# Kernel optimization log

Hardware: AMD Instinct MI355X
Metric: run time of the kernel (lower is better)

The kernel has to match this reference:

```python
import jax, jax.numpy as jnp
import numpy as np


def setup_inputs() -> dict:
    key = jax.random.key(0)
    ks = jax.random.split(key, 15)
    B, r, d, h, na = 64, 64, 2048, 64, 256
    x = jax.random.normal(ks[0], (B, d, na), dtype=jnp.float32)
    L = jax.random.randint(ks[1], (B, 2, na), 0, 2).astype(jnp.float32)
    p = lambda i, shp: jax.random.normal(ks[i], shp, dtype=jnp.float32)
    return {
        "x": x, "L": L,
        "Aq": p(2, (r, d)), "Ak": p(3, (r, d)), "Av": p(4, (r, d)),
        "Aq1": p(5, (r, r)), "Ak1": p(6, (r, r)), "Av1": p(7, (r, r)),
        "Aq5": p(8, (r, r)), "Ak5": p(9, (r, r)), "Av5": p(10, (r, r)),
        "Ao": p(11, (r, r)), "Ao1": p(12, (r, r)), "Ao5": p(13, (h, r)),
    }


def reference(x, L, Aq, Ak, Av, Aq1, Ak1, Av1, Aq5, Ak5, Av5, Ao, Ao1, Ao5):
    B, d, na = x.shape
    # numNeighbors: count of L[:,0,:] >= 1 per batch, +1 -> [B,1,1]
    numN = jnp.sum((L[:, 0, :] >= 1.0).astype(jnp.float32), axis=1)[:, None, None] + 1.0
    scale = jnp.sqrt(numN)  # [B,1,1]

    def attn(M, Wq, Wk, Wv):
        # M: [B, f, na]; Wq/Wk/Wv: [r, f]
        Q = jax.nn.sigmoid(jnp.einsum('rf,bfn->bnr', Wq, M))  # [B,na,r]
        K = jax.nn.sigmoid(jnp.einsum('rf,bfn->brn', Wk, M))  # [B,r,na]
        V = jax.nn.sigmoid(jnp.einsum('rf,bfn->bnr', Wv, M))  # [B,na,r]
        A = jax.nn.softmax(jnp.einsum('bnr,brm->bnm', Q, K) / scale, axis=2)
        return jnp.einsum('bnm,bmr->brn', A, V)  # [B,r,na]

    o = attn(x, Aq, Ak, Av)
    M = jax.nn.silu(jnp.einsum('sr,brn->bsn', Ao, o))
    o = attn(M, Aq1, Ak1, Av1)
    M = jax.nn.silu(jnp.einsum('sr,brn->bsn', Ao1, o))
    o = attn(M, Aq5, Ak5, Av5)
    M = jax.nn.silu(jnp.einsum('hr,brn->bhn', Ao5, o))  # [B,h,na]

    blk = d // na  # rows per block (8)
    def diagvec(i):
        # kron(sum-of-squares, ones(1,2)) == repeat each element twice -> [B, 2*na]
        return jnp.repeat(jnp.sum(M[:, i * blk:(i + 1) * blk, :] ** 2, axis=1), 2, axis=1)

    M11, M12, M21, M22 = diagvec(0), diagvec(1), diagvec(2), diagvec(3)
    Mpp = jnp.sum(M[:, 4 * blk:, :] ** 2, axis=1)  # [B, na]

    # q = x[:, :4, :].transpose(1,2).reshape(B, 4*na) (agent-major ordering)
    q = jnp.transpose(x[:, :4, :], (0, 2, 1)).reshape(B, 4 * na)
    q1, q2 = q[:, :2 * na], q[:, 2 * na:]
    # Block matrix [[diag(M11), diag(M12)], [diag(M21), diag(M22)]] quadratic form,
    # computed without materializing the [B, 4na, 4na] matrix.
    quad = jnp.sum(M11 * q1 * q1 + M12 * q1 * q2 + M21 * q2 * q1 + M22 * q2 * q2,
                   axis=1, keepdims=True)
    return quad + jnp.sum(Mpp, axis=1, keepdims=True)  # [B, 1]
```

## Files before the change

### kernel.cpp

```cpp
#include <hip/hip_runtime.h>
#include <stdint.h>

typedef _Float16 f16;
typedef f16 f16x8 __attribute__((ext_vector_type(8)));
typedef float f32x4 __attribute__((ext_vector_type(4)));

#define MFMA(a,b,c) __builtin_amdgcn_mfma_f32_16x16x32_f16(a, b, c, 0, 0, 0)

__device__ __forceinline__ float sigmoidf_(float z) { return 1.0f / (1.0f + __expf(-z)); }

__global__ void prep_kernel(const float* __restrict__ L,
    const float* __restrict__ Aq, const float* __restrict__ Ak, const float* __restrict__ Av,
    const float* __restrict__ Aq1, const float* __restrict__ Ak1, const float* __restrict__ Av1,
    const float* __restrict__ Aq5, const float* __restrict__ Ak5, const float* __restrict__ Av5,
    const float* __restrict__ Ao, const float* __restrict__ Ao1, const float* __restrict__ Ao5,
    float* __restrict__ scale, f16* __restrict__ Wcat, f16* __restrict__ Wsm,
    float* __restrict__ out)
{
  __shared__ float r4[4];
  int blk = blockIdx.x, t = threadIdx.x;
  if (blk < 64) {
    float v = (L[blk * 512 + t] >= 1.0f) ? 1.0f : 0.0f;
    #pragma unroll
    for (int off = 32; off; off >>= 1) v += __shfl_down(v, off);
    if ((t & 63) == 0) r4[t >> 6] = v;
    __syncthreads();
    if (t == 0) scale[blk] = sqrtf(r4[0] + r4[1] + r4[2] + r4[3] + 1.0f);
  } else if (blk < 160) {
    int base = (blk - 64) * 4096;
    for (int i = 0; i < 16; i++) {
      int idx = base + t + i * 256;
      int row = idx >> 11, col = idx & 2047;
      float v = (row < 64) ? Aq[row * 2048 + col]
              : (row < 128) ? Ak[(row - 64) * 2048 + col]
              : Av[(row - 128) * 2048 + col];
      Wcat[idx] = (f16)v;
    }
  } else if (blk < 169) {
    int j = blk - 160;
    const float* s = (j == 0) ? Aq1 : (j == 1) ? Ak1 : (j == 2) ? Av1 : (j == 3) ? Aq5
                   : (j == 4) ? Ak5 : (j == 5) ? Av5 : (j == 6) ? Ao : (j == 7) ? Ao1 : Ao5;
    for (int i = 0; i < 16; i++) { int idx = t + i * 256; Wsm[j * 4096 + idx] = (f16)s[idx]; }
  } else {
    if (t < 64) out[t] = 0.0f;
  }
}

__global__ __launch_bounds__(256) void qkv1_kernel(const float* __restrict__ x,
    const f16* __restrict__ Wcat, f16* __restrict__ Qt, f16* __restrict__ Kt,
    f16* __restrict__ Vg)
{
  int b = blockIdx.y, n0 = blockIdx.x * 32;
  int t = threadIdx.x, lane = t & 63, w = t >> 6;
  int l15 = lane & 15, q = lane >> 4;
  __shared__ f16 xt[32 * 72];
  __shared__ f16 wt[192 * 72];
  f32x4 acc[2][3] = {};
  const float* xb = x + (size_t)b * 524288 + n0;
  int tn = t & 31, fg = t >> 5;

  for (int f0 = 0; f0 < 2048; f0 += 64) {
    #pragma unroll
    for (int rep = 0; rep < 4; rep++) {
      int fl = fg * 8 + rep * 2;
      float a0 = xb[(size_t)(f0 + fl) * 256 + tn];
      float a1 = xb[(size_t)(f0 + fl + 1) * 256 + tn];
      uint32_t pk = (uint32_t)__builtin_bit_cast(uint16_t, (f16)a0)
                  | ((uint32_t)__builtin_bit_cast(uint16_t, (f16)a1) << 16);
      *(uint32_t*)&xt[tn * 72 + fl] = pk;
    }
    #pragma unroll
    for (int i = 0; i < 6; i++) {
      int id = t + i * 256, r = id >> 3, c = id & 7;
      *(uint4*)&wt[r * 72 + c * 8] = *(const uint4*)(Wcat + (size_t)r * 2048 + f0 + c * 8);
    }
    __syncthreads();
    #pragma unroll
    for (int ks = 0; ks < 2; ks++) {
      int k0 = ks * 32 + q * 8;
      f16x8 af[2], bf[3];
      af[0] = *(const f16x8*)&xt[l15 * 72 + k0];
      af[1] = *(const f16x8*)&xt[(16 + l15) * 72 + k0];
      #pragma unroll
      for (int j = 0; j < 3; j++) bf[j] = *(const f16x8*)&wt[((w * 3 + j) * 16 + l15) * 72 + k0];
      #pragma unroll
      for (int nt = 0; nt < 2; nt++)
        #pragma unroll
        for (int j = 0; j < 3; j++)
          acc[nt][j] = MFMA(af[nt], bf[j], acc[nt][j]);
    }
    __syncthreads();
  }
  #pragma unroll
  for (int nt = 0; nt < 2; nt++)
    #pragma unroll
    for (int j = 0; j < 3; j++) {
      int rr = (w * 3 + j) * 16 + l15;
      float s[4];
      #pragma unroll
      for (int reg = 0; reg < 4; reg++) s[reg] = sigmoidf_(acc[nt][j][reg]);
      int nbase = n0 + nt * 16 + q * 4;
      if (rr < 64) {
        #pragma unroll
        for (int reg = 0; reg < 4; reg++)
          Qt[(size_t)b * 16384 + (size_t)(nbase + reg) * 64 + rr] = (f16)s[reg];
      } else if (rr < 128) {
        #pragma unroll
        for (int reg = 0; reg < 4; reg++)
          Kt[(size_t)b * 16384 + (size_t)(nbase + reg) * 64 + (rr - 64)] = (f16)s[reg];
      } else {
        union { f16 h[4]; uint2 u; } pk;
        #pragma unroll
        for (int reg = 0; reg < 4; reg++) pk.h[reg] = (f16)s[reg];
        *(uint2*)(Vg + (size_t)b * 16384 + (size_t)(rr - 128) * 256 + nbase) = pk.u;
      }
    }
}

template<int LAYER>
__global__ __launch_bounds__(512) void attnB_kernel(const float* __restrict__ x,
    const float* __restrict__ scale, const f16* __restrict__ Wsm,
    const f16* __restrict__ Qtg, const f16* __restrict__ Ktg, const f16* __restrict__ Vgg,
    const f16* __restrict__ Min, f16* __restrict__ Mout, float* __restrict__ out)
{
  int g = blockIdx.x, b = blockIdx.y, n0 = g * 64;
  int t = threadIdx.x, lane = t & 63, w = t >> 6;
  int l15 = lane & 15, q = lane >> 4;
  __shared__ f16 KT[256 * 72];
  __shared__ f16 SM[256 * 72];
  __shared__ f16 VM[64 * 264];
  __shared__ f16 QT[64 * 72];
  __shared__ f16 OT[64 * 72];
  __shared__ float denomS[64];

  float sinv = 1.0f / scale[b];
  if (t < 64) denomS[t] = 0.0f;

  if (LAYER == 0) {
    const uint4* qs = (const uint4*)(Qtg + (size_t)b * 16384 + (size_t)n0 * 64);
    { int n = t >> 3, c = t & 7; *(uint4*)&QT[n * 72 + c * 8] = qs[t]; }
    const uint4* ks = (const uint4*)(Ktg + (size_t)b * 16384);
    const uint4* vs = (const uint4*)(Vgg + (size_t)b * 16384);
    #pragma unroll
    for (int i = 0; i < 4; i++) {
      int id = t + i * 512;
      int m = id >> 3, c = id & 7;
      *(uint4*)&KT[m * 72 + c * 8] = ks[id];
      int r = id >> 5, c2 = id & 31;
      *(uint4*)&VM[r * 264 + c2 * 8] = vs[id];
    }
  } else {
    const uint4* ms = (const uint4*)(Min + (size_t)b * 16384);
    #pragma unroll
    for (int i = 0; i < 4; i++) {
      int id = t + i * 512, m = id >> 3, c = id & 7;
      *(uint4*)&SM[m * 72 + c * 8] = ms[id];
    }
  }
  __syncthreads();

  const f16* Wq = Wsm + (size_t)(LAYER == 1 ? 0 : 3) * 4096;
  const f16* Wk = Wsm + (size_t)(LAYER == 1 ? 1 : 4) * 4096;
  const f16* Wv = Wsm + (size_t)(LAYER == 1 ? 2 : 5) * 4096;
  const f16* Wo = Wsm + (size_t)(LAYER == 0 ? 6 : (LAYER == 1 ? 7 : 8)) * 4096;

  if (LAYER > 0) {
    if (w < 4) {
      f16x8 bk[4][2];
      #pragma unroll
      for (int rt = 0; rt < 4; rt++) {
        bk[rt][0] = *(const f16x8*)(Wk + (rt * 16 + l15) * 64 + q * 8);
        bk[rt][1] = *(const f16x8*)(Wk + (rt * 16 + l15) * 64 + 32 + q * 8);
      }
      #pragma unroll
      for (int mi = 0; mi < 4; mi++) {
        int mt = w * 4 + mi;
        f16x8 a0 = *(const f16x8*)&SM[(mt * 16 + l15) * 72 + q * 8];
        f16x8 a1 = *(const f16x8*)&SM[(mt * 16 + l15) * 72 + 32 + q * 8];
        #pragma unroll
        for (int rt = 0; rt < 4; rt++) {
          f32x4 acc = {}; acc = MFMA(a0, bk[rt][0], acc); acc = MFMA(a1, bk[rt][1], acc);
          #pragma unroll
          for (int reg = 0; reg < 4; reg++)
            KT[(mt * 16 + q * 4 + reg) * 72 + rt * 16 + l15] = (f16)sigmoidf_(acc[reg]);
        }
      }
    } else {
      f16x8 av[4][2];
      #pragma unroll
      for (int rt = 0; rt < 4; rt++) {
        av[rt][0] = *(const f16x8*)(Wv + (rt * 16 + l15) * 64 + q * 8);
        av[rt][1] = *(const f16x8*)(Wv + (rt * 16 + l15) * 64 + 32 + q * 8);
      }
      #pragma unroll
      for (int mi = 0; mi < 4; mi++) {
        int mt = (w - 4) * 4 + mi;
        f16x8 b0 = *(const f16x8*)&SM[(mt * 16 + l15) * 72 + q * 8];
        f16x8 b1 = *(const f16x8*)&SM[(mt * 16 + l15) * 72 + 32 + q * 8];
        #pragma unroll
        for (int rt = 0; rt < 4; rt++) {
          f32x4 acc = {}; acc = MFMA(av[rt][0], b0, acc); acc = MFMA(av[rt][1], b1, acc);
          #pragma unroll
          for (int reg = 0; reg < 4; reg++)
            VM[(rt * 16 + q * 4 + reg) * 264 + mt * 16 + l15] = (f16)sigmoidf_(acc[reg]);
        }
      }
    }
    {
      int nt = w >> 1;
      f16x8 a0 = *(const f16x8*)&SM[(n0 + nt * 16 + l15) * 72 + q * 8];
      f16x8 a1 = *(const f16x8*)&SM[(n0 + nt * 16 + l15) * 72 + 32 + q * 8];
      #pragma unroll
      for (int j = 0; j < 2; j++) {
        int rt = (w & 1) * 2 + j;
        f16x8 b0 = *(const f16x8*)(Wq + (rt * 16 + l15) * 64 + q * 8);
        f16x8 b1 = *(const f16x8*)(Wq + (rt * 16 + l15) * 64 + 32 + q * 8);
        f32x4 acc = {}; acc = MFMA(a0, b0, acc); acc = MFMA(a1, b1, acc);
        #pragma unroll
        for (int reg = 0; reg < 4; reg++)
          QT[(nt * 16 + q * 4 + reg) * 72 + rt * 16 + l15] = (f16)sigmoidf_(acc[reg]);
      }
    }
    __syncthreads();
  }

  {
    int nt = w >> 1;
    f16x8 a0 = *(const f16x8*)&QT[(nt * 16 + l15) * 72 + q * 8];
    f16x8 a1 = *(const f16x8*)&QT[(nt * 16 + l15) * 72 + 32 + q * 8];
    float dsum[4] = {0.f, 0.f, 0.f, 0.f};
    #pragma unroll
    for (int mi = 0; mi < 8; mi++) {
      int mt = (w & 1) * 8 + mi;
      f16x8 b0 = *(const f16x8*)&KT[(mt * 16 + l15) * 72 + q * 8];
      f16x8 b1 = *(const f16x8*)&KT[(mt * 16 + l15) * 72 + 32 + q * 8];
      f32x4 acc = {}; acc = MFMA(a0, b0, acc); acc = MFMA(a1, b1, acc);
      #pragma unroll
      for (int reg = 0; reg < 4; reg++) {
        float e = __expf(acc[reg] * sinv);
        dsum[reg] += e;
        SM[(nt * 16 + q * 4 + reg) * 264 + mt * 16 + l15] = (f16)e;
      }
    }
    #pragma unroll
    for (int reg = 0; reg < 4; reg++) {
      #pragma unroll
      for (int mask = 1; mask < 16; mask <<= 1) dsum[reg] += __shfl_xor(dsum[reg], mask);
    }
    if (l15 == 0) {
      #pragma unroll
      for (int reg = 0; reg < 4; reg++) atomicAdd(&denomS[nt * 16 + q * 4 + reg], dsum[reg]);
    }
  }
  __syncthreads();

  {
    int nt = w >> 1;
    f32x4 oacc[2] = {};
    #pragma unroll
    for (int kc = 0; kc < 8; kc++) {
      f16x8 af = *(const f16x8*)&SM[(nt * 16 + l15) * 264 + kc * 32 + q * 8];
      #pragma unroll
      for (int j = 0; j < 2; j++) {
        int rt = (w & 1) * 2 + j;
        f16x8 bf = *(const f16x8*)&VM[(rt * 16 + l15) * 264 + kc * 32 + q * 8];
        oacc[j] = MFMA(af, bf, oacc[j]);
      }
    }
    #pragma unroll
    for (int j = 0; j < 2; j++) {
      int rt = (w & 1) * 2 + j;
      #pragma unroll
      for (int reg = 0; reg < 4; reg++) {
        int row = nt * 16 + q * 4 + reg;
        OT[row * 72 + rt * 16 + l15] = (f16)(oacc[j][reg] / denomS[row]);
      }
    }
  }
  __syncthreads();

  f16* Mst = QT;
  {
    int nt = w >> 1;
    f16x8 a0 = *(const f16x8*)&OT[(nt * 16 + l15) * 72 + q * 8];
    f16x8 a1 = *(const f16x8*)&OT[(nt * 16 + l15) * 72 + 32 + q * 8];
    #pragma unroll
    for (int j = 0; j < 2; j++) {
      int st = (w & 1) * 2 + j;
      f16x8 b0 = *(const f16x8*)(Wo + (st * 16 + l15) * 64 + q * 8);
      f16x8 b1 = *(const f16x8*)(Wo + (st * 16 + l15) * 64 + 32 + q * 8);
      f32x4 acc = {}; acc = MFMA(a0, b0, acc); acc = MFMA(a1, b1, acc);
      #pragma unroll
      for (int reg = 0; reg < 4; reg++) {
        float z = acc[reg];
        Mst[(nt * 16 + q * 4 + reg) * 64 + st * 16 + l15] = (f16)(z * sigmoidf_(z));
      }
    }
  }
  __syncthreads();

  if (LAYER < 2) {
    int row = t >> 3, c = t & 7;
    *(uint4*)(Mout + (size_t)b * 16384 + (size_t)(n0 + row) * 64 + c * 8)
        = *(const uint4*)&Mst[row * 64 + c * 8];
  } else {
    float contrib = 0.0f;
    if (t < 64) {
      int ntok = n0 + t;
      const f16* row = &Mst[t * 64];
      float d[4] = {0, 0, 0, 0}, pp = 0.0f;
      #pragma unroll
      for (int gg = 0; gg < 8; gg++) {
        f16x8 v = *(const f16x8*)(row + gg * 8);
        float ss = 0.0f;
        #pragma unroll
        for (int k = 0; k < 8; k++) { float f = (float)v[k]; ss += f * f; }
        if (gg < 4) d[gg] = ss; else pp += ss;
      }
      int np = ntok >> 1, c0 = (ntok & 1) * 2;
      const float* xb = x + (size_t)b * 524288 + (size_t)c0 * 256;
      float q1a = xb[np], q1b = xb[256 + np];
      float q2a = xb[128 + np], q2b = xb[384 + np];
      contrib = d[0] * (q1a * q1a + q1b * q1b)
              + (d[1] + d[2]) * (q1a * q2a + q1b * q2b)
              + d[3] * (q2a * q2a + q2b * q2b) + pp;
    }
    if (w == 0) {
      #pragma unroll
      for (int off = 32; off; off >>= 1) contrib += __shfl_down(contrib, off);
      if (lane == 0) atomicAdd(out + b, contrib);
    }
  }
}

extern "C" void kernel_launch(void* const* d_in, const int* in_sizes, int n_in,
                              void* d_out, int out_size, void* d_ws, size_t ws_size,
                              hipStream_t stream) {
  const float* x   = (const float*)d_in[0];
  const float* L   = (const float*)d_in[1];
  const float* Aq  = (const float*)d_in[2];
  const float* Ak  = (const float*)d_in[3];
  const float* Av  = (const float*)d_in[4];
  const float* Aq1 = (const float*)d_in[5];
  const float* Ak1 = (const float*)d_in[6];
  const float* Av1 = (const float*)d_in[7];
  const float* Aq5 = (const float*)d_in[8];
  const float* Ak5 = (const float*)d_in[9];
  const float* Av5 = (const float*)d_in[10];
  const float* Ao  = (const float*)d_in[11];
  const float* Ao1 = (const float*)d_in[12];
  const float* Ao5 = (const float*)d_in[13];

  char* ws = (char*)d_ws;
  float* scale = (float*)ws;
  f16* Wcat  = (f16*)(ws + 256);
  f16* Wsm   = (f16*)(ws + 786688);
  f16* Qtg   = (f16*)(ws + 860416);
  f16* Ktg   = (f16*)(ws + 2957568);
  f16* Vgg   = (f16*)(ws + 5054720);
  f16* MbufA = (f16*)(ws + 7151872);
  f16* MbufB = (f16*)(ws + 9249024);
  float* out = (float*)d_out;

  prep_kernel<<<170, 256, 0, stream>>>(L, Aq, Ak, Av, Aq1, Ak1, Av1,
                                       Aq5, Ak5, Av5, Ao, Ao1, Ao5, scale, Wcat, Wsm, out);
  qkv1_kernel<<<dim3(8, 64), 256, 0, stream>>>(x, Wcat, Qtg, Ktg, Vgg);
  attnB_kernel<0><<<dim3(4, 64), 512, 0, stream>>>(x, scale, Wsm, Qtg, Ktg, Vgg,
                                                   nullptr, MbufA, out);
  attnB_kernel<1><<<dim3(4, 64), 512, 0, stream>>>(x, scale, Wsm, Qtg, Ktg, Vgg,
                                                   MbufA, MbufB, out);
  attnB_kernel<2><<<dim3(4, 64), 512, 0, stream>>>(x, scale, Wsm, Qtg, Ktg, Vgg,
                                                   MbufB, nullptr, out);
}
```

Baseline: 272.1 us.

## Fuse three attention layers with per-batch grid barriers and LDS-free QKV GEMM

Merges the three per-layer attention launches into one persistent kernel that loops over layers and synchronises the four blocks of each batch through a global atomic counter with spin-waiting. Separately, the first QKV projection drops its shared-memory staging: weights are pre-permuted in the prep kernel into the MFMA fragment layout, and x is gathered directly into registers. This targets launch overhead and LDS/barrier costs. The trade-offs are reliance on all blocks being co-resident for the spin barrier, and less coalesced strided global loads of x.

```diff
diff --git a/kernel.cpp b/kernel.cpp
--- a/kernel.cpp
+++ b/kernel.cpp
@@ -14,8 +14,8 @@
     const float* __restrict__ Aq1, const float* __restrict__ Ak1, const float* __restrict__ Av1,
     const float* __restrict__ Aq5, const float* __restrict__ Ak5, const float* __restrict__ Av5,
     const float* __restrict__ Ao, const float* __restrict__ Ao1, const float* __restrict__ Ao5,
-    float* __restrict__ scale, f16* __restrict__ Wcat, f16* __restrict__ Wsm,
-    float* __restrict__ out)
+    float* __restrict__ scale, f16* __restrict__ Wopt, f16* __restrict__ Wsm,
+    float* __restrict__ out, unsigned int* __restrict__ flagg)
 {
   __shared__ float r4[4];
   int blk = blockIdx.x, t = threadIdx.x;
@@ -30,11 +30,12 @@
     int base = (blk - 64) * 4096;
     for (int i = 0; i < 16; i++) {
       int idx = base + t + i * 256;
-      int row = idx >> 11, col = idx & 2047;
-      float v = (row < 64) ? Aq[row * 2048 + col]
-              : (row < 128) ? Ak[(row - 64) * 2048 + col]
-              : Av[(row - 128) * 2048 + col];
-      Wcat[idx] = (f16)v;
+      int r = idx >> 11, k = idx & 2047;
+      float v = (r < 64) ? Aq[r * 2048 + k]
+              : (r < 128) ? Ak[(r - 64) * 2048 + k]
+              : Av[(r - 128) * 2048 + k];
+      int rt = r >> 4, lr = r & 15, kc = k >> 5, qq = (k >> 3) & 3, jj = k & 7;
+      Wopt[((rt * 64 + kc) * 16 + lr) * 32 + qq * 8 + jj] = (f16)v;
     }
   } else if (blk < 169) {
     int j = blk - 160;
@@ -43,54 +44,43 @@
     for (int i = 0; i < 16; i++) { int idx = t + i * 256; Wsm[j * 4096 + idx] = (f16)s[idx]; }
   } else {
     if (t < 64) out[t] = 0.0f;
+    else if (t < 128) flagg[t - 64] = 0u;
   }
 }
 
 __global__ __launch_bounds__(256) void qkv1_kernel(const float* __restrict__ x,
-    const f16* __restrict__ Wcat, f16* __restrict__ Qt, f16* __restrict__ Kt,
+    const f16* __restrict__ Wopt, f16* __restrict__ Qt, f16* __restrict__ Kt,
     f16* __restrict__ Vg)
 {
   int b = blockIdx.y, n0 = blockIdx.x * 32;
   int t = threadIdx.x, lane = t & 63, w = t >> 6;
   int l15 = lane & 15, q = lane >> 4;
-  __shared__ f16 xt[32 * 72];
-  __shared__ f16 wt[192 * 72];
   f32x4 acc[2][3] = {};
-  const float* xb = x + (size_t)b * 524288 + n0;
-  int tn = t & 31, fg = t >> 5;
-
-  for (int f0 = 0; f0 < 2048; f0 += 64) {
-    #pragma unroll
-    for (int rep = 0; rep < 4; rep++) {
-      int fl = fg * 8 + rep * 2;
-      float a0 = xb[(size_t)(f0 + fl) * 256 + tn];
-      float a1 = xb[(size_t)(f0 + fl + 1) * 256 + tn];
-      uint32_t pk = (uint32_t)__builtin_bit_cast(uint16_t, (f16)a0)
-                  | ((uint32_t)__builtin_bit_cast(uint16_t, (f16)a1) << 16);
-      *(uint32_t*)&xt[tn * 72 + fl] = pk;
-    }
-    #pragma unroll
-    for (int i = 0; i < 6; i++) {
-      int id = t + i * 256, r = id >> 3, c = id & 7;
-      *(uint4*)&wt[r * 72 + c * 8] = *(const uint4*)(Wcat + (size_t)r * 2048 + f0 + c * 8);
-    }
-    __syncthreads();
-    #pragma unroll
-    for (int ks = 0; ks < 2; ks++) {
-      int k0 = ks * 32 + q * 8;
-      f16x8 af[2], bf[3];
-      af[0] = *(const f16x8*)&xt[l15 * 72 + k0];
-      af[1] = *(const f16x8*)&xt[(16 + l15) * 72 + k0];
-      #pragma unroll
-      for (int j = 0; j < 3; j++) bf[j] = *(const f16x8*)&wt[((w * 3 + j) * 16 + l15) * 72 + k0];
-      #pragma unroll
-      for (int nt = 0; nt < 2; nt++)
-        #pragma unroll
-        for (int j = 0; j < 3; j++)
-          acc[nt][j] = MFMA(af[nt], bf[j], acc[nt][j]);
-    }
-    __syncthreads();
+  const float* xb0 = x + (size_t)b * 524288 + n0 + l15;
+  const float* xb1 = xb0 + 16;
+  const f16* wb = Wopt + ((size_t)(w * 3) * 1024 + l15) * 32 + q * 8;
+
+  #pragma unroll 2
+  for (int kc = 0; kc < 64; kc++) {
+    int f = kc * 32 + q * 8;
+    const float* p0 = xb0 + (size_t)f * 256;
+    const float* p1 = xb1 + (size_t)f * 256;
+    f16x8 af0, af1;
+    #pragma unroll
+    for (int j = 0; j < 8; j++) af0[j] = (f16)p0[j * 256];
+    #pragma unroll
+    for (int j = 0; j < 8; j++) af1[j] = (f16)p1[j * 256];
+    f16x8 bf[3];
+    #pragma unroll
+    for (int j = 0; j < 3; j++)
+      bf[j] = *(const f16x8*)(wb + (size_t)j * 32768 + kc * 512);
+    #pragma unroll
+    for (int j = 0; j < 3; j++) {
+      acc[0][j] = MFMA(af0, bf[j], acc[0][j]);
+      acc[1][j] = MFMA(af1, bf[j], acc[1][j]);
+    }
   }
+
   #pragma unroll
   for (int nt = 0; nt < 2; nt++)
     #pragma unroll
@@ -117,11 +107,11 @@
     }
 }
 
-template<int LAYER>
-__global__ __launch_bounds__(512) void attnB_kernel(const float* __restrict__ x,
+__global__ __launch_bounds__(512) void attn_fused(const float* __restrict__ x,
     const float* __restrict__ scale, const f16* __restrict__ Wsm,
     const f16* __restrict__ Qtg, const f16* __restrict__ Ktg, const f16* __restrict__ Vgg,
-    const f16* __restrict__ Min, f16* __restrict__ Mout, float* __restrict__ out)
+    f16* __restrict__ MA, f16* __restrict__ MB,
+    unsigned int* __restrict__ flagg, float* __restrict__ out)
 {
   int g = blockIdx.x, b = blockIdx.y, n0 = g * 64;
   int t = threadIdx.x, lane = t & 63, w = t >> 6;
@@ -134,201 +124,214 @@
   __shared__ float denomS[64];
 
   float sinv = 1.0f / scale[b];
-  if (t < 64) denomS[t] = 0.0f;
-
-  if (LAYER == 0) {
-    const uint4* qs = (const uint4*)(Qtg + (size_t)b * 16384 + (size_t)n0 * 64);
-    { int n = t >> 3, c = t & 7; *(uint4*)&QT[n * 72 + c * 8] = qs[t]; }
-    const uint4* ks = (const uint4*)(Ktg + (size_t)b * 16384);
-    const uint4* vs = (const uint4*)(Vgg + (size_t)b * 16384);
-    #pragma unroll
-    for (int i = 0; i < 4; i++) {
-      int id = t + i * 512;
-      int m = id >> 3, c = id & 7;
-      *(uint4*)&KT[m * 72 + c * 8] = ks[id];
-      int r = id >> 5, c2 = id & 31;
-      *(uint4*)&VM[r * 264 + c2 * 8] = vs[id];
-    }
-  } else {
-    const uint4* ms = (const uint4*)(Min + (size_t)b * 16384);
-    #pragma unroll
-    for (int i = 0; i < 4; i++) {
-      int id = t + i * 512, m = id >> 3, c = id & 7;
-      *(uint4*)&SM[m * 72 + c * 8] = ms[id];
-    }
-  }
-  __syncthreads();
-
-  const f16* Wq = Wsm + (size_t)(LAYER == 1 ? 0 : 3) * 4096;
-  const f16* Wk = Wsm + (size_t)(LAYER == 1 ? 1 : 4) * 4096;
-  const f16* Wv = Wsm + (size_t)(LAYER == 1 ? 2 : 5) * 4096;
-  const f16* Wo = Wsm + (size_t)(LAYER == 0 ? 6 : (LAYER == 1 ? 7 : 8)) * 4096;
-
-  if (LAYER > 0) {
-    if (w < 4) {
-      f16x8 bk[4][2];
-      #pragma unroll
-      for (int rt = 0; rt < 4; rt++) {
-        bk[rt][0] = *(const f16x8*)(Wk + (rt * 16 + l15) * 64 + q * 8);
-        bk[rt][1] = *(const f16x8*)(Wk + (rt * 16 + l15) * 64 + 32 + q * 8);
-      }
-      #pragma unroll
-      for (int mi = 0; mi < 4; mi++) {
-        int mt = w * 4 + mi;
-        f16x8 a0 = *(const f16x8*)&SM[(mt * 16 + l15) * 72 + q * 8];
-        f16x8 a1 = *(const f16x8*)&SM[(mt * 16 + l15) * 72 + 32 + q * 8];
+
+  #pragma unroll 1
+  for (int l = 0; l < 3; l++) {
+    if (t < 64) denomS[t] = 0.0f;
+
+    const f16* Wq = Wsm + (size_t)(l == 1 ? 0 : 3) * 4096;
+    const f16* Wk = Wsm + (size_t)(l == 1 ? 1 : 4) * 4096;
+    const f16* Wv = Wsm + (size_t)(l == 1 ? 2 : 5) * 4096;
+    const f16* Wo = Wsm + (size_t)(l == 0 ? 6 : (l == 1 ? 7 : 8)) * 4096;
+
+    if (l == 0) {
+      const uint4* qs = (const uint4*)(Qtg + (size_t)b * 16384 + (size_t)n0 * 64);
+      { int n = t >> 3, c = t & 7; *(uint4*)&QT[n * 72 + c * 8] = qs[t]; }
+      const uint4* ks = (const uint4*)(Ktg + (size_t)b * 16384);
+      const uint4* vs = (const uint4*)(Vgg + (size_t)b * 16384);
+      #pragma unroll
+      for (int i = 0; i < 4; i++) {
+        int id = t + i * 512;
+        int m = id >> 3, c = id & 7;
+        *(uint4*)&KT[m * 72 + c * 8] = ks[id];
+        int r = id >> 5, c2 = id & 31;
+        *(uint4*)&VM[r * 264 + c2 * 8] = vs[id];
+      }
+      __syncthreads();
+    } else {
+      const f16* Min = (l == 1) ? MA : MB;
+      const uint4* ms = (const uint4*)(Min + (size_t)b * 16384);
+      #pragma unroll
+      for (int i = 0; i < 4; i++) {
+        int id = t + i * 512, m = id >> 3, c = id & 7;
+        *(uint4*)&SM[m * 72 + c * 8] = ms[id];
+      }
+      __syncthreads();
+      if (w < 4) {
+        f16x8 bk[4][2];
         #pragma unroll
         for (int rt = 0; rt < 4; rt++) {
-          f32x4 acc = {}; acc = MFMA(a0, bk[rt][0], acc); acc = MFMA(a1, bk[rt][1], acc);
+          bk[rt][0] = *(const f16x8*)(Wk + (rt * 16 + l15) * 64 + q * 8);
+          bk[rt][1] = *(const f16x8*)(Wk + (rt * 16 + l15) * 64 + 32 + q * 8);
+        }
+        #pragma unroll
+        for (int mi = 0; mi < 4; mi++) {
+          int mt = w * 4 + mi;
+          f16x8 a0 = *(const f16x8*)&SM[(mt * 16 + l15) * 72 + q * 8];
+          f16x8 a1 = *(const f16x8*)&SM[(mt * 16 + l15) * 72 + 32 + q * 8];
+          #pragma unroll
+          for (int rt = 0; rt < 4; rt++) {
+            f32x4 acc = {}; acc = MFMA(a0, bk[rt][0], acc); acc = MFMA(a1, bk[rt][1], acc);
+            #pragma unroll
+            for (int reg = 0; reg < 4; reg++)
+              KT[(mt * 16 + q * 4 + reg) * 72 + rt * 16 + l15] = (f16)sigmoidf_(acc[reg]);
+          }
+        }
+      } else {
+        f16x8 av[4][2];
+        #pragma unroll
+        for (int rt = 0; rt < 4; rt++) {
+          av[rt][0] = *(const f16x8*)(Wv + (rt * 16 + l15) * 64 + q * 8);
+          av[rt][1] = *(const f16x8*)(Wv + (rt * 16 + l15) * 64 + 32 + q * 8);
+        }
+        #pragma unroll
+        for (int mi = 0; mi < 4; mi++) {
+          int mt = (w - 4) * 4 + mi;
+          f16x8 b0 = *(const f16x8*)&SM[(mt * 16 + l15) * 72 + q * 8];
+          f16x8 b1 = *(const f16x8*)&SM[(mt * 16 + l15) * 72 + 32 + q * 8];
+          #pragma unroll
+          for (int rt = 0; rt < 4; rt++) {
+            f32x4 acc = {}; acc = MFMA(av[rt][0], b0, acc); acc = MFMA(av[rt][1], b1, acc);
+            #pragma unroll
+            for (int reg = 0; reg < 4; reg++)
+              VM[(rt * 16 + q * 4 + reg) * 264 + mt * 16 + l15] = (f16)sigmoidf_(acc[reg]);
+          }
+        }
+      }
+      {
+        int nt = w >> 1;
+        f16x8 a0 = *(const f16x8*)&SM[(n0 + nt * 16 + l15) * 72 + q * 8];
+        f16x8 a1 = *(const f16x8*)&SM[(n0 + nt * 16 + l15) * 72 + 32 + q * 8];
+        #pragma unroll
+        for (int j = 0; j < 2; j++) {
+          int rt = (w & 1) * 2 + j;
+          f16x8 b0 = *(const f16x8*)(Wq + (rt * 16 + l15) * 64 + q * 8);
+          f16x8 b1 = *(const f16x8*)(Wq + (rt * 16 + l15) * 64 + 32 + q * 8);
+          f32x4 acc = {}; acc = MFMA(a0, b0, acc); acc = MFMA(a1, b1, acc);
           #pragma unroll
           for (int reg = 0; reg < 4; reg++)
-            KT[(mt * 16 + q * 4 + reg) * 72 + rt * 16 + l15] = (f16)sigmoidf_(acc[reg]);
-        }
-      }
-    } else {
-      f16x8 av[4][2];
-      #pragma unroll
-      for (int rt = 0; rt < 4; rt++) {
-        av[rt][0] = *(const f16x8*)(Wv + (rt * 16 + l15) * 64 + q * 8);
-        av[rt][1] = *(const f16x8*)(Wv + (rt * 16 + l15) * 64 + 32 + q * 8);
-      }
-      #pragma unroll
-      for (int mi = 0; mi < 4; mi++) {
-        int mt = (w - 4) * 4 + mi;
-        f16x8 b0 = *(const f16x8*)&SM[(mt * 16 + l15) * 72 + q * 8];
-        f16x8 b1 = *(const f16x8*)&SM[(mt * 16 + l15) * 72 + 32 + q * 8];
-        #pragma unroll
-        for (int rt = 0; rt < 4; rt++) {
-          f32x4 acc = {}; acc = MFMA(av[rt][0], b0, acc); acc = MFMA(av[rt][1], b1, acc);
-          #pragma unroll
-          for (int reg = 0; reg < 4; reg++)
-            VM[(rt * 16 + q * 4 + reg) * 264 + mt * 16 + l15] = (f16)sigmoidf_(acc[reg]);
-        }
-      }
-    }
+            QT[(nt * 16 + q * 4 + reg) * 72 + rt * 16 + l15] = (f16)sigmoidf_(acc[reg]);
+        }
+      }
+      __syncthreads();
+    }
+
     {
       int nt = w >> 1;
-      f16x8 a0 = *(const f16x8*)&SM[(n0 + nt * 16 + l15) * 72 + q * 8];
-      f16x8 a1 = *(const f16x8*)&SM[(n0 + nt * 16 + l15) * 72 + 32 + q * 8];
+      f16x8 a0 = *(const f16x8*)&QT[(nt * 16 + l15) * 72 + q * 8];
+      f16x8 a1 = *(const f16x8*)&QT[(nt * 16 + l15) * 72 + 32 + q * 8];
+      float dsum[4] = {0.f, 0.f, 0.f, 0.f};
+      #pragma unroll
+      for (int mi = 0; mi < 8; mi++) {
+        int mt = (w & 1) * 8 + mi;
+        f16x8 b0 = *(const f16x8*)&KT[(mt * 16 + l15) * 72 + q * 8];
+        f16x8 b1 = *(const f16x8*)&KT[(mt * 16 + l15) * 72 + 32 + q * 8];
+        f32x4 acc = {}; acc = MFMA(a0, b0, acc); acc = MFMA(a1, b1, acc);
+        #pragma unroll
+        for (int reg = 0; reg < 4; reg++) {
+          float e = __expf(acc[reg] * sinv);
+          dsum[reg] += e;
+          SM[(nt * 16 + q * 4 + reg) * 264 + mt * 16 + l15] = (f16)e;
+        }
+      }
+      #pragma unroll
+      for (int reg = 0; reg < 4; reg++) {
+        #pragma unroll
+        for (int mask = 1; mask < 16; mask <<= 1) dsum[reg] += __shfl_xor(dsum[reg], mask);
+      }
+      if (l15 == 0) {
+        #pragma unroll
+        for (int reg = 0; reg < 4; reg++) atomicAdd(&denomS[nt * 16 + q * 4 + reg], dsum[reg]);
+      }
+    }
+    __syncthreads();
+
+    {
+      int nt = w >> 1;
+      f32x4 oacc[2] = {};
+      #pragma unroll
+      for (int kc = 0; kc < 8; kc++) {
+        f16x8 af = *(const f16x8*)&SM[(nt * 16 + l15) * 264 + kc * 32 + q * 8];
+        #pragma unroll
+        for (int j = 0; j < 2; j++) {
+          int rt = (w & 1) * 2 + j;
+          f16x8 bf = *(const f16x8*)&VM[(rt * 16 + l15) * 264 + kc * 32 + q * 8];
+          oacc[j] = MFMA(af, bf, oacc[j]);
+        }
+      }
       #pragma unroll
       for (int j = 0; j < 2; j++) {
         int rt = (w & 1) * 2 + j;
-        f16x8 b0 = *(const f16x8*)(Wq + (rt * 16 + l15) * 64 + q * 8);
-        f16x8 b1 = *(const f16x8*)(Wq + (rt * 16 + l15) * 64 + 32 + q * 8);
+        #pragma unroll
+        for (int reg = 0; reg < 4; reg++) {
+          int row = nt * 16 + q * 4 + reg;
+          OT[row * 72 + rt * 16 + l15] = (f16)(oacc[j][reg] / denomS[row]);
+        }
+      }
+    }
+    __syncthreads();
+
+    f16* Mst = QT;
+    {
+      int nt = w >> 1;
+      f16x8 a0 = *(const f16x8*)&OT[(nt * 16 + l15) * 72 + q * 8];
+      f16x8 a1 = *(const f16x8*)&OT[(nt * 16 + l15) * 72 + 32 + q * 8];
+      #pragma unroll
+      for (int j = 0; j < 2; j++) {
+        int st = (w & 1) * 2 + j;
+        f16x8 b0 = *(const f16x8*)(Wo + (st * 16 + l15) * 64 + q * 8);
+        f16x8 b1 = *(const f16x8*)(Wo + (st * 16 + l15) * 64 + 32 + q * 8);
         f32x4 acc = {}; acc = MFMA(a0, b0, acc); acc = MFMA(a1, b1, acc);
         #pragma unroll
-        for (int reg = 0; reg < 4; reg++)
-          QT[(nt * 16 + q * 4 + reg) * 72 + rt * 16 + l15] = (f16)sigmoidf_(acc[reg]);
+        for (int reg = 0; reg < 4; reg++) {
+          float z = acc[reg];
+          Mst[(nt * 16 + q * 4 + reg) * 64 + st * 16 + l15] = (f16)(z * sigmoidf_(z));
+        }
       }
     }
     __syncthreads();
-  }
-
-  {
-    int nt = w >> 1;
-    f16x8 a0 = *(const f16x8*)&QT[(nt * 16 + l15) * 72 + q * 8];
-    f16x8 a1 = *(const f16x8*)&QT[(nt * 16 + l15) * 72 + 32 + q * 8];
-    float dsum[4] = {0.f, 0.f, 0.f, 0.f};
-    #pragma unroll
-    for (int mi = 0; mi < 8; mi++) {
-      int mt = (w & 1) * 8 + mi;
-      f16x8 b0 = *(const f16x8*)&KT[(mt * 16 + l15) * 72 + q * 8];
-      f16x8 b1 = *(const f16x8*)&KT[(mt * 16 + l15) * 72 + 32 + q * 8];
-      f32x4 acc = {}; acc = MFMA(a0, b0, acc); acc = MFMA(a1, b1, acc);
-      #pragma unroll
-      for (int reg = 0; reg < 4; reg++) {
-        float e = __expf(acc[reg] * sinv);
-        dsum[reg] += e;
-        SM[(nt * 16 + q * 4 + reg) * 264 + mt * 16 + l15] = (f16)e;
-      }
-    }
-    #pragma unroll
-    for (int reg = 0; reg < 4; reg++) {
-      #pragma unroll
-      for (int mask = 1; mask < 16; mask <<= 1) dsum[reg] += __shfl_xor(dsum[reg], mask);
-    }
-    if (l15 == 0) {
-      #pragma unroll
-      for (int reg = 0; reg < 4; reg++) atomicAdd(&denomS[nt * 16 + q * 4 + reg], dsum[reg]);
-    }
-  }
-  __syncthreads();
-
-  {
-    int nt = w >> 1;
-    f32x4 oacc[2] = {};
-    #pragma unroll
-    for (int kc = 0; kc < 8; kc++) {
-      f16x8 af = *(const f16x8*)&SM[(nt * 16 + l15) * 264 + kc * 32 + q * 8];
-      #pragma unroll
-      for (int j = 0; j < 2; j++) {
-        int rt = (w & 1) * 2 + j;
-        f16x8 bf = *(const f16x8*)&VM[(rt * 16 + l15) * 264 + kc * 32 + q * 8];
-        oacc[j] = MFMA(af, bf, oacc[j]);
-      }
-    }
-    #pragma unroll
-    for (int j = 0; j < 2; j++) {
-      int rt = (w & 1) * 2 + j;
-      #pragma unroll
-      for (int reg = 0; reg < 4; reg++) {
-        int row = nt * 16 + q * 4 + reg;
-        OT[row * 72 + rt * 16 + l15] = (f16)(oacc[j][reg] / denomS[row]);
-      }
-    }
-  }
-  __syncthreads();
-
-  f16* Mst = QT;
-  {
-    int nt = w >> 1;
-    f16x8 a0 = *(const f16x8*)&OT[(nt * 16 + l15) * 72 + q * 8];
-    f16x8 a1 = *(const f16x8*)&OT[(nt * 16 + l15) * 72 + 32 + q * 8];
-    #pragma unroll
-    for (int j = 0; j < 2; j++) {
-      int st = (w & 1) * 2 + j;
-      f16x8 b0 = *(const f16x8*)(Wo + (st * 16 + l15) * 64 + q * 8);
-      f16x8 b1 = *(const f16x8*)(Wo + (st * 16 + l15) * 64 + 32 + q * 8);
-      f32x4 acc = {}; acc = MFMA(a0, b0, acc); acc = MFMA(a1, b1, acc);
-      #pragma unroll
-      for (int reg = 0; reg < 4; reg++) {
-        float z = acc[reg];
-        Mst[(nt * 16 + q * 4 + reg) * 64 + st * 16 + l15] = (f16)(z * sigmoidf_(z));
-      }
-    }
-  }
-  __syncthreads();
-
-  if (LAYER < 2) {
-    int row = t >> 3, c = t & 7;
-    *(uint4*)(Mout + (size_t)b * 16384 + (size_t)(n0 + row) * 64 + c * 8)
-        = *(const uint4*)&Mst[row * 64 + c * 8];
-  } else {
-    float contrib = 0.0f;
-    if (t < 64) {
-      int ntok = n0 + t;
-      const f16* row = &Mst[t * 64];
-      float d[4] = {0, 0, 0, 0}, pp = 0.0f;
-      #pragma unroll
-      for (int gg = 0; gg < 8; gg++) {
-        f16x8 v = *(const f16x8*)(row + gg * 8);
-        float ss = 0.0f;
-        #pragma unroll
-        for (int k = 0; k < 8; k++) { float f = (float)v[k]; ss += f * f; }
-        if (gg < 4) d[gg] = ss; else pp += ss;
-      }
-      int np = ntok >> 1, c0 = (ntok & 1) * 2;
-      const float* xb = x + (size_t)b * 524288 + (size_t)c0 * 256;
-      float q1a = xb[np], q1b = xb[256 + np];
-      float q2a = xb[128 + np], q2b = xb[384 + np];
-      contrib = d[0] * (q1a * q1a + q1b * q1b)
-              + (d[1] + d[2]) * (q1a * q2a + q1b * q2b)
-              + d[3] * (q2a * q2a + q2b * q2b) + pp;
-    }
-    if (w == 0) {
-      #pragma unroll
-      for (int off = 32; off; off >>= 1) contrib += __shfl_down(contrib, off);
-      if (lane == 0) atomicAdd(out + b, contrib);
+
+    if (l < 2) {
+      f16* Mout = (l == 0) ? MA : MB;
+      int row = t >> 3, c = t & 7;
+      *(uint4*)(Mout + (size_t)b * 16384 + (size_t)(n0 + row) * 64 + c * 8)
+          = *(const uint4*)&Mst[row * 64 + c * 8];
+      if (t == 0) {
+        __threadfence();
+        atomicAdd(&flagg[b], 1u);
+        unsigned int target = 4u * (unsigned)(l + 1);
+        while (__hip_atomic_load(&flagg[b], __ATOMIC_ACQUIRE, __HIP_MEMORY_SCOPE_AGENT) < target)
+          __builtin_amdgcn_s_sleep(2);
+        __threadfence();
+      }
+      __syncthreads();
+    } else {
+      float contrib = 0.0f;
+      if (t < 64) {
+        int ntok = n0 + t;
+        const f16* row = &Mst[t * 64];
+        float d[4] = {0, 0, 0, 0}, pp = 0.0f;
+        #pragma unroll
+        for (int gg = 0; gg < 8; gg++) {
+          f16x8 v = *(const f16x8*)(row + gg * 8);
+          float ss = 0.0f;
+          #pragma unroll
+          for (int k = 0; k < 8; k++) { float f = (float)v[k]; ss += f * f; }
+          if (gg < 4) d[gg] = ss; else pp += ss;
+        }
+        int np = ntok >> 1, c0 = (ntok & 1) * 2;
+        const float* xb = x + (size_t)b * 524288 + (size_t)c0 * 256;
+        float q1a = xb[np], q1b = xb[256 + np];
+        float q2a = xb[128 + np], q2b = xb[384 + np];
+        contrib = d[0] * (q1a * q1a + q1b * q1b)
+                + (d[1] + d[2]) * (q1a * q2a + q1b * q2b)
+                + d[3] * (q2a * q2a + q2b * q2b) + pp;
+      }
+      if (w == 0) {
+        #pragma unroll
+        for (int off = 32; off; off >>= 1) contrib += __shfl_down(contrib, off);
+        if (lane == 0) atomicAdd(out + b, contrib);
+      }
     }
   }
 }
@@ -353,22 +356,20 @@
 
   char* ws = (char*)d_ws;
   float* scale = (float*)ws;
-  f16* Wcat  = (f16*)(ws + 256);
+  f16* Wopt  = (f16*)(ws + 256);
   f16* Wsm   = (f16*)(ws + 786688);
   f16* Qtg   = (f16*)(ws + 860416);
   f16* Ktg   = (f16*)(ws + 2957568);
   f16* Vgg   = (f16*)(ws + 5054720);
   f16* MbufA = (f16*)(ws + 7151872);
   f16* MbufB = (f16*)(ws + 9249024);
+  unsigned int* flagg = (unsigned int*)(ws + 11346176);
   float* out = (float*)d_out;
 
   prep_kernel<<<170, 256, 0, stream>>>(L, Aq, Ak, Av, Aq1, Ak1, Av1,
-                                       Aq5, Ak5, Av5, Ao, Ao1, Ao5, scale, Wcat, Wsm, out);
-  qkv1_kernel<<<dim3(8, 64), 256, 0, stream>>>(x, Wcat, Qtg, Ktg, Vgg);
-  attnB_kernel<0><<<dim3(4, 64), 512, 0, stream>>>(x, scale, Wsm, Qtg, Ktg, Vgg,
-                                                   nullptr, MbufA, out);
-  attnB_kernel<1><<<dim3(4, 64), 512, 0, stream>>>(x, scale, Wsm, Qtg, Ktg, Vgg,
-                                                   MbufA, MbufB, out);
-  attnB_kernel<2><<<dim3(4, 64), 512, 0, stream>>>(x, scale, Wsm, Qtg, Ktg, Vgg,
-                                                   MbufB, nullptr, out);
+                                       Aq5, Ak5, Av5, Ao, Ao1, Ao5,
+                                       scale, Wopt, Wsm, out, flagg);
+  qkv1_kernel<<<dim3(8, 64), 256, 0, stream>>>(x, Wopt, Qtg, Ktg, Vgg);
+  attn_fused<<<dim3(4, 64), 512, 0, stream>>>(x, scale, Wsm, Qtg, Ktg, Vgg,
+                                              MbufA, MbufB, flagg, out);
 }
```

Result: slower. 333.6 us (+22.6%).
